# Kernel optimization log

Hardware: AMD Instinct MI355X
Metric: run time of the kernel (lower is better)

The kernel has to match this reference:

```python
import jax, jax.numpy as jnp
import numpy as np

B, S, E, H, D = 4, 2048, 1024, 16, 64


def setup_inputs() -> dict:
    key = jax.random.key(0)
    ks = jax.random.split(key, 6)
    scale_in = 1.0 / np.sqrt(E)
    return {
        "x": jax.random.normal(ks[0], (B, S, E), dtype=jnp.float32),
        "Wq": jax.random.normal(ks[1], (H, E, D), dtype=jnp.float32) * scale_in,
        "bq": jnp.zeros((H, D), dtype=jnp.float32),
        "Wk": jax.random.normal(ks[2], (H, E, D), dtype=jnp.float32) * scale_in,
        "bk": jnp.zeros((H, D), dtype=jnp.float32),
        "Wv": jax.random.normal(ks[3], (H, E, D), dtype=jnp.float32) * scale_in,
        "bv": jnp.zeros((H, D), dtype=jnp.float32),
        "Wo": jax.random.normal(ks[4], (H * D, E), dtype=jnp.float32) * (1.0 / np.sqrt(H * D)),
        "bo": jnp.zeros((E,), dtype=jnp.float32),
    }


def reference(x, Wq, bq, Wk, bk, Wv, bv, Wo, bo):
    # Per-head Q/K/V projections, batched over heads: [B,S,E] x [H,E,D] -> [B,H,S,D]
    q = jnp.einsum("bse,hed->bhsd", x, Wq) + bq[None, :, None, :]
    k = jnp.einsum("bse,hed->bhsd", x, Wk) + bk[None, :, None, :]
    v = jnp.einsum("bse,hed->bhsd", x, Wv) + bv[None, :, None, :]

    d = q.shape[-1]
    scores = jnp.einsum("bhqd,bhkd->bhqk", q, k) / jnp.sqrt(jnp.asarray(d, q.dtype))
    # Causal mask (registered tril buffer of size max_seq_len in HeadAttention)
    seq = scores.shape[-1]
    causal = jnp.tril(jnp.ones((seq, seq), dtype=bool))
    scores = jnp.where(causal[None, None, :, :], scores, jnp.asarray(-1e9, scores.dtype))
    attn = jax.nn.softmax(scores, axis=-1)
    out = jnp.einsum("bhqk,bhkd->bhqd", attn, v)  # [B,H,S,D]

    # Concat heads: [B,S,H*D], then output projection (dropout is identity in eval)
    out = out.transpose(0, 2, 1, 3).reshape(out.shape[0], out.shape[2], -1)
    return out @ Wo + bo
```

## Files before the change

kernel.cpp:

```cpp
#include <hip/hip_runtime.h>

typedef __bf16 bf16x8 __attribute__((ext_vector_type(8)));
typedef __bf16 bf16x4 __attribute__((ext_vector_type(4)));
typedef float  f32x4  __attribute__((ext_vector_type(4)));

#define B_    4
#define S_    2048
#define E_    1024
#define H_    16
#define D_    64
#define MROWS (B_*S_)

#define SCORE_SCALE 0.18033688011112043f

__device__ __forceinline__ void load_lds16(const void* g, void* l) {
  __builtin_amdgcn_global_load_lds((__attribute__((address_space(1))) void*)g,
                                   (__attribute__((address_space(3))) void*)l,
                                   16, 0, 0);
}

__device__ __forceinline__ f32x4 mfma16(bf16x8 a, bf16x8 b, f32x4 c) {
  return __builtin_amdgcn_mfma_f32_16x16x32_bf16(a, b, c, 0, 0, 0);
}

__device__ __forceinline__ int swz(int row, int dchunk) {
  return row * 64 + ((dchunk ^ (row & 7)) * 8);
}


__global__ void prep(const float4* __restrict__ x, const float* __restrict__ Wq,
                     const float* __restrict__ Wk, const float* __restrict__ Wv,
                     const float* __restrict__ bq, const float* __restrict__ bk,
                     const float* __restrict__ bv, const float* __restrict__ Wo,
                     __bf16* __restrict__ xb, __bf16* __restrict__ Wt,
                     float* __restrict__ bqkv, __bf16* __restrict__ Wot) {
  __shared__ float t[64][65];
  int bid = blockIdx.x;
  if (bid < 8192) {
    int id = bid * 256 + threadIdx.x;
    float4 v = x[id];
    bf16x4 o = { (__bf16)v.x, (__bf16)v.y, (__bf16)v.z, (__bf16)v.w };
    *(bf16x4*)(xb + 4 * (size_t)id) = o;
    return;
  }
  int tx = threadIdx.x & 63;
  int ty = threadIdx.x >> 6;
  if (bid < 8960) {
    int b2 = bid - 8192;
    int e0 = (b2 & 15) * 64;
    int h  = (b2 >> 4) & 15;
    int p  = b2 >> 8;
    const float* W    = (p == 0) ? Wq : (p == 1) ? Wk : Wv;
    const float* bsrc = (p == 0) ? bq : (p == 1) ? bk : bv;
#pragma unroll
    for (int r = 0; r < 16; ++r) {
      int eL = ty + r * 4;
      t[eL][tx] = W[((size_t)h * 1024 + (e0 + eL)) * 64 + tx];
    }
    __syncthreads();
#pragma unroll
    for (int r = 0; r < 16; ++r) {
      int d = ty + r * 4;
      Wt[((size_t)(p * 1024 + h * 64 + d)) * 1024 + e0 + tx] = (__bf16)t[tx][d];
    }
    if ((b2 & 15) == 0 && threadIdx.x < 64)
      bqkv[p * 1024 + h * 64 + threadIdx.x] = bsrc[h * 64 + threadIdx.x];
  } else {
    int b2 = bid - 8960;
    int hd0 = (b2 >> 4) * 64;
    int e0  = (b2 & 15) * 64;
#pragma unroll
    for (int r = 0; r < 16; ++r) {
      int hdL = ty + r * 4;
      t[hdL][tx] = Wo[(size_t)(hd0 + hdL) * 1024 + e0 + tx];
    }
    __syncthreads();
#pragma unroll
    for (int r = 0; r < 16; ++r) {
      int eL = ty + r * 4;
      Wot[(size_t)(e0 + eL) * 1024 + hd0 + tx] = (__bf16)t[tx][eL];
    }
  }
}


template <int MODE, int BN, int NDIM>
__global__ __launch_bounds__(512, 4) void gemm8h(const __bf16* __restrict__ A,
                                                 const __bf16* __restrict__ Bt,
                                                 const float* __restrict__ bias,
                                                 void* __restrict__ Cout,
                                                 __bf16* __restrict__ VT) {
  constexpr int K = 1024;
  constexpr int NB = BN / 64;
  constexpr int WC = BN / 4;
  __shared__ __attribute__((aligned(16))) __bf16 As[2 * 128 * 64];
  __shared__ __attribute__((aligned(16))) __bf16 Bs[2 * BN * 64];

  int tid = threadIdx.x, wave = tid >> 6, lane = tid & 63;
  int quad = lane >> 4, cc = lane & 15;
  constexpr int nb = NDIM / BN;
  int nwg = (int)gridDim.x;
  int bid = (int)blockIdx.x;
  bid = (bid & 7) * (nwg >> 3) + (bid >> 3);
  int bm = bid / nb, bn = bid % nb;
  const __bf16* Abase = A + (size_t)bm * 128 * K;
  const __bf16* Bbase = Bt + (size_t)bn * BN * K;
  int wrow = (wave >> 2) * 64;
  int wcol = (wave & 3) * WC;

  f32x4 acc[4][NB];
#pragma unroll
  for (int m = 0; m < 4; ++m)
#pragma unroll
    for (int n = 0; n < NB; ++n) acc[m][n] = (f32x4){0.f, 0.f, 0.f, 0.f};

  int srl = tid >> 3;
  int sch = tid & 7;
  int scol = (sch ^ (srl & 7)) * 8;

#define STAGE_A(t, sub, buf)                                                   \
  load_lds16(Abase + (size_t)((sub) * 64 + srl) * K + (t) * 64 + scol,         \
             &As[(buf) * 8192 + (sub) * 4096 + tid * 8])
#define STAGE_B(t, sub, buf)                                                   \
  load_lds16(Bbase + (size_t)((sub) * 64 + srl) * K + (t) * 64 + scol,         \
             &Bs[(buf) * (BN * 64) + (sub) * 4096 + tid * 8])

#pragma unroll
  for (int s = 0; s < 2; ++s) STAGE_A(0, s, 0);
#pragma unroll
  for (int s = 0; s < NB; ++s) STAGE_B(0, s, 0);
#pragma unroll
  for (int s = 0; s < 2; ++s) STAGE_A(1, s, 1);
  asm volatile("s_waitcnt vmcnt(2)" ::: "memory");
  __builtin_amdgcn_sched_barrier(0);
  asm volatile("s_barrier" ::: "memory");

  bf16x8 af[4][2], bfr[NB][2];

#define RD_B(buf)                                                              \
  _Pragma("unroll") for (int n = 0; n < NB; ++n)                               \
      _Pragma("unroll") for (int kk = 0; kk < 2; ++kk)                         \
          bfr[n][kk] = *(const bf16x8*)&Bs[(buf) * (BN * 64) +                 \
                                           swz(wcol + n * 16 + cc, kk * 4 + quad)]
#define RD_A2(buf, mlo)                                                        \
  _Pragma("unroll") for (int m = mlo; m < (mlo) + 2; ++m)                      \
      _Pragma("unroll") for (int kk = 0; kk < 2; ++kk)                         \
          af[m][kk] = *(const bf16x8*)&As[(buf) * 8192 +                       \
                                          swz(wrow + m * 16 + cc, kk * 4 + quad)]
#define MFMA_M(m)                                                              \
  do {                                                                         \
    __builtin_amdgcn_s_setprio(1);                                             \
    _Pragma("unroll") for (int n = 0; n < NB; ++n)                             \
        _Pragma("unroll") for (int kk = 0; kk < 2; ++kk)                       \
            acc[m][n] = mfma16(af[m][kk], bfr[n][kk], acc[m][n]);              \
    __builtin_amdgcn_s_setprio(0);                                             \
  } while (0)
#define LGKM0                                                                  \
  asm volatile("s_waitcnt lgkmcnt(0)" ::: "memory");                           \
  __builtin_amdgcn_sched_barrier(0)
#define VMC2                                                                   \
  asm volatile("s_waitcnt vmcnt(2)" ::: "memory");                             \
  __builtin_amdgcn_sched_barrier(0)
#define BAR asm volatile("s_barrier" ::: "memory")

#pragma unroll 1
  for (int it = 0; it < 8; ++it) {
    int b_t = 2 * it + 1;
    int c_t = (2 * it + 2) & 15;
    int d_t = (2 * it + 3) & 15;
    RD_B(0); RD_A2(0, 0);
    STAGE_B(b_t, 0, 1); STAGE_B(b_t, 1, 1);
    LGKM0; MFMA_M(0); BAR;
    RD_A2(0, 2);
    if (NB >= 3) STAGE_B(b_t, 2, 1);
    LGKM0; MFMA_M(1); BAR;
    STAGE_A(c_t, 0, 0); STAGE_A(c_t, 1, 0);
    MFMA_M(2); BAR;
    MFMA_M(3);
    VMC2; BAR;
    RD_B(1); RD_A2(1, 0);
    STAGE_B(c_t, 0, 0); STAGE_B(c_t, 1, 0);
    LGKM0; MFMA_M(0); BAR;
    RD_A2(1, 2);
    if (NB >= 3) STAGE_B(c_t, 2, 0);
    LGKM0; MFMA_M(1); BAR;
    STAGE_A(d_t, 0, 1); STAGE_A(d_t, 1, 1);
    MFMA_M(2); BAR;
    MFMA_M(3);
    VMC2; BAR;
  }
  asm volatile("s_waitcnt vmcnt(0)" ::: "memory");

#pragma unroll
  for (int n = 0; n < NB; ++n) {
    int gcol = bn * BN + wcol + n * 16 + cc;
    float bv = bias[gcol];
#pragma unroll
    for (int m = 0; m < 4; ++m) {
      int grow0 = bm * 128 + wrow + m * 16 + quad * 4;
      if (MODE == 0) {
#pragma unroll
        for (int r = 0; r < 4; ++r)
          ((float*)Cout)[(size_t)(grow0 + r) * NDIM + gcol] = acc[m][n][r] + bv;
      } else if (gcol < 2048) {
        float sc = (gcol < 1024) ? SCORE_SCALE : 1.0f;
#pragma unroll
        for (int r = 0; r < 4; ++r)
          ((__bf16*)Cout)[(size_t)(grow0 + r) * 2048 + gcol] =
              (__bf16)((acc[m][n][r] + bv) * sc);
      } else {
        int bh = (grow0 >> 11) * 16 + ((gcol >> 6) & 15);
        int d  = gcol & 63;
        bf16x4 pk;
#pragma unroll
        for (int r = 0; r < 4; ++r) pk[r] = (__bf16)(acc[m][n][r] + bv);
        *(bf16x4*)&VT[((size_t)(bh * 64 + d)) * 2048 + (grow0 & 2047)] = pk;
      }
    }
  }
#undef STAGE_A
#undef STAGE_B
#undef RD_B
#undef RD_A2
#undef MFMA_M
#undef LGKM0
#undef VMC2
#undef BAR
}


__global__ __launch_bounds__(256, 3) void attn(const __bf16* __restrict__ QKb,
                                               const __bf16* __restrict__ VT,
                                               __bf16* __restrict__ O) {
  int bx = blockIdx.x;
  int bh = bx & 63;
  int g  = bx >> 6;
  int qt = (g < 8) ? (15 - g) : (g - 8);
  int h  = bh & 15;
  int b  = bh >> 4;
  int q0 = qt * 128;
  int tid = threadIdx.x, wave = tid >> 6, lane = tid & 63;
  int quad = lane >> 4, c = lane & 15;

  __shared__ __attribute__((aligned(16))) __bf16 smem[24576];
  __bf16* Qs = smem;
  __bf16* Ks = smem + 8192;
  __bf16* Vs = smem + 16384;
  __bf16* Ps = smem + wave * 2048;

  const __bf16* Qbase = QKb + (size_t)(b * S_ + q0) * 2048 + h * 64;
  const __bf16* Vbase = VT + (size_t)bh * (64 * 2048);
#pragma unroll
  for (int p = 0; p < 4; ++p) {
    int gi = tid + p * 256;
    int row = gi >> 3, pch = gi & 7;
    load_lds16(Qbase + (size_t)row * 2048 + (pch ^ (row & 7)) * 8, &Qs[gi * 8]);
  }
  {
    const __bf16* Kb = QKb + (size_t)(b * S_) * 2048 + 1024 + h * 64;
#pragma unroll
    for (int p = 0; p < 2; ++p) {
      int gi = tid + p * 256;
      int row = gi >> 3, pch = gi & 7;
      load_lds16(Kb + (size_t)row * 2048 + (pch ^ (row & 7)) * 8, &Ks[gi * 8]);
      load_lds16(Vbase + (size_t)row * 2048 + (pch ^ (row & 7)) * 8, &Vs[gi * 8]);
    }
  }
  __syncthreads();

  bf16x8 qf[2][2];
#pragma unroll
  for (int i = 0; i < 2; ++i)
#pragma unroll
    for (int kk = 0; kk < 2; ++kk)
      qf[i][kk] = *(const bf16x8*)&Qs[swz(wave * 32 + i * 16 + c, kk * 4 + quad)];

  const __bf16 one_b = (__bf16)1.0f;
  bf16x8 ones = { one_b, one_b, one_b, one_b, one_b, one_b, one_b, one_b };

  f32x4 acc_o[2][4], acc_l[2];
#pragma unroll
  for (int i = 0; i < 2; ++i) {
    acc_l[i] = (f32x4){0.f, 0.f, 0.f, 0.f};
#pragma unroll
    for (int j = 0; j < 4; ++j) acc_o[i][j] = (f32x4){0.f, 0.f, 0.f, 0.f};
  }

  int qwave = q0 + wave * 32;
  int ntiles = qt * 2 + 2;
  for (int t = 0; t < ntiles; ++t) {
    int cur = t & 1;
    if (t + 1 < ntiles) {
      int kv1 = (t + 1) * 64;
      const __bf16* Kb = QKb + (size_t)(b * S_ + kv1) * 2048 + 1024 + h * 64;
      const __bf16* Vb = Vbase + kv1;
#pragma unroll
      for (int p = 0; p < 2; ++p) {
        int gi = tid + p * 256;
        int row = gi >> 3, pch = gi & 7;
        load_lds16(Kb + (size_t)row * 2048 + (pch ^ (row & 7)) * 8,
                   &Ks[(cur ^ 1) * 4096 + gi * 8]);
        load_lds16(Vb + (size_t)row * 2048 + (pch ^ (row & 7)) * 8,
                   &Vs[(cur ^ 1) * 4096 + gi * 8]);
      }
    }

    int kv0 = t * 64;
    if (kv0 <= qwave + 31) {
      const __bf16* Kc = Ks + cur * 4096;
      const __bf16* Vc = Vs + cur * 4096;

      f32x4 acc_t[2][4];
#pragma unroll
      for (int i = 0; i < 2; ++i)
#pragma unroll
        for (int j = 0; j < 4; ++j) acc_t[i][j] = (f32x4){0.f, 0.f, 0.f, 0.f};
      bf16x8 kf[4][2];
#pragma unroll
      for (int j = 0; j < 4; ++j)
#pragma unroll
        for (int kk = 0; kk < 2; ++kk)
          kf[j][kk] = *(const bf16x8*)&Kc[swz(j * 16 + c, kk * 4 + quad)];
      __builtin_amdgcn_s_setprio(1);
#pragma unroll
      for (int i = 0; i < 2; ++i)
#pragma unroll
        for (int j = 0; j < 4; ++j)
#pragma unroll
          for (int kk = 0; kk < 2; ++kk)
            acc_t[i][j] = mfma16(kf[j][kk], qf[i][kk], acc_t[i][j]);
      __builtin_amdgcn_s_setprio(0);

      bool domask = (kv0 + 63 > qwave);
#pragma unroll
      for (int i = 0; i < 2; ++i) {
        int q_l = i * 16 + c;
        int q_g = qwave + q_l;
#pragma unroll
        for (int j = 0; j < 4; ++j) {
          bf16x4 pk;
#pragma unroll
          for (int r = 0; r < 4; ++r) {
            float p = __builtin_amdgcn_exp2f(acc_t[i][j][r]);
            if (domask) {
              int kv = kv0 + j * 16 + quad * 4 + r;
              p = (kv > q_g) ? 0.f : p;
            }
            pk[r] = (__bf16)p;
          }
          int dch8 = j * 2 + (quad >> 1);
          int phys = q_l * 64 + ((dch8 ^ (q_l & 7)) * 8) + (quad & 1) * 4;
          *(bf16x4*)&Ps[phys] = pk;
        }
      }

      bf16x8 pf[2][2], vf[4][2];
#pragma unroll
      for (int i = 0; i < 2; ++i)
#pragma unroll
        for (int kk = 0; kk < 2; ++kk)
          pf[i][kk] = *(const bf16x8*)&Ps[swz(i * 16 + c, kk * 4 + quad)];
#pragma unroll
      for (int j = 0; j < 4; ++j)
#pragma unroll
        for (int kk = 0; kk < 2; ++kk)
          vf[j][kk] = *(const bf16x8*)&Vc[swz(j * 16 + c, kk * 4 + quad)];
      __builtin_amdgcn_s_setprio(1);
#pragma unroll
      for (int i = 0; i < 2; ++i) {
#pragma unroll
        for (int j = 0; j < 4; ++j)
#pragma unroll
          for (int kk = 0; kk < 2; ++kk)
            acc_o[i][j] = mfma16(pf[i][kk], vf[j][kk], acc_o[i][j]);
        acc_l[i] = mfma16(pf[i][0], ones, acc_l[i]);
        acc_l[i] = mfma16(pf[i][1], ones, acc_l[i]);
      }
      __builtin_amdgcn_s_setprio(0);
    }

    __syncthreads();
  }

  __bf16* Obase = O + (size_t)(b * S_ + q0) * 1024 + h * 64;
#pragma unroll
  for (int i = 0; i < 2; ++i)
#pragma unroll
    for (int r = 0; r < 4; ++r) {
      float rl = 1.0f / acc_l[i][r];
      int row = wave * 32 + i * 16 + quad * 4 + r;
#pragma unroll
      for (int j = 0; j < 4; ++j)
        Obase[(size_t)row * 1024 + j * 16 + c] = (__bf16)(acc_o[i][j][r] * rl);
    }
}


extern "C" void kernel_launch(void* const* d_in, const int* in_sizes, int n_in,
                              void* d_out, int out_size, void* d_ws, size_t ws_size,
                              hipStream_t stream) {
  (void)in_sizes; (void)n_in; (void)out_size; (void)ws_size;
  const float* x  = (const float*)d_in[0];
  const float* Wq = (const float*)d_in[1];
  const float* bq = (const float*)d_in[2];
  const float* Wk = (const float*)d_in[3];
  const float* bk = (const float*)d_in[4];
  const float* Wv = (const float*)d_in[5];
  const float* bv = (const float*)d_in[6];
  const float* Wo = (const float*)d_in[7];
  const float* bo = (const float*)d_in[8];

  char* w = (char*)d_ws;
  __bf16* xb   = (__bf16*)(w);
  __bf16* Wt   = (__bf16*)(w + (16ull << 20));
  __bf16* Wot  = (__bf16*)(w + (22ull << 20));
  float*  bqkv = (float*) (w + (24ull << 20));
  __bf16* QKb  = (__bf16*)(w + (25ull << 20));
  __bf16* Ob   = (__bf16*)(w + (57ull << 20));
  __bf16* VT   = (__bf16*)(w + (73ull << 20));

  prep<<<9216, 256, 0, stream>>>((const float4*)x, Wq, Wk, Wv, bq, bk, bv, Wo,
                                 xb, Wt, bqkv, Wot);
  gemm8h<1, 192, 3072><<<1024, 512, 0, stream>>>(xb, Wt, bqkv, (void*)QKb, VT);
  attn<<<1024, 256, 0, stream>>>(QKb, VT, Ob);
  gemm8h<0, 128, 1024><<<512, 512, 0, stream>>>(Ob, Wot, bo, d_out, nullptr);
}
```

Baseline: 242.5 us.

## Pair high and low causal query tiles in one 512-thread attention block

Each attention block now processes two 128-row query tiles, one near the end and its mirror near the start, with 8 waves sharing a single K/V stream through LDS. This halves the K/V global loads per query pair and balances causal work inside each block instead of across blocks. The trade-offs are more LDS per block, fewer blocks (512 instead of 1024), and waves on the low tile sitting idle for the later K/V tiles while still joining the barriers.

```diff
diff --git a/kernel.cpp b/kernel.cpp
--- a/kernel.cpp
+++ b/kernel.cpp
@@ -229,42 +229,42 @@
 }
 
 
-__global__ __launch_bounds__(256, 3) void attn(const __bf16* __restrict__ QKb,
+__global__ __launch_bounds__(512, 4) void attn(const __bf16* __restrict__ QKb,
                                                const __bf16* __restrict__ VT,
                                                __bf16* __restrict__ O) {
   int bx = blockIdx.x;
   int bh = bx & 63;
   int g  = bx >> 6;
-  int qt = (g < 8) ? (15 - g) : (g - 8);
+  int qth = 15 - g;
+  int qtl = g;
   int h  = bh & 15;
   int b  = bh >> 4;
-  int q0 = qt * 128;
+  int q0h = qth * 128, q0l = qtl * 128;
   int tid = threadIdx.x, wave = tid >> 6, lane = tid & 63;
   int quad = lane >> 4, c = lane & 15;
 
-  __shared__ __attribute__((aligned(16))) __bf16 smem[24576];
+  __shared__ __attribute__((aligned(16))) __bf16 smem[32768];
   __bf16* Qs = smem;
-  __bf16* Ks = smem + 8192;
-  __bf16* Vs = smem + 16384;
+  __bf16* Ks = smem + 16384;
+  __bf16* Vs = smem + 24576;
   __bf16* Ps = smem + wave * 2048;
 
-  const __bf16* Qbase = QKb + (size_t)(b * S_ + q0) * 2048 + h * 64;
+  const __bf16* Qbh = QKb + (size_t)(b * S_ + q0h) * 2048 + h * 64;
+  const __bf16* Qbl = QKb + (size_t)(b * S_ + q0l) * 2048 + h * 64;
   const __bf16* Vbase = VT + (size_t)bh * (64 * 2048);
 #pragma unroll
   for (int p = 0; p < 4; ++p) {
-    int gi = tid + p * 256;
+    int gi = tid + p * 512;
     int row = gi >> 3, pch = gi & 7;
-    load_lds16(Qbase + (size_t)row * 2048 + (pch ^ (row & 7)) * 8, &Qs[gi * 8]);
+    const __bf16* base = (p < 2) ? Qbh : Qbl;
+    load_lds16(base + (size_t)(row & 127) * 2048 + (pch ^ (row & 7)) * 8,
+               &Qs[gi * 8]);
   }
   {
     const __bf16* Kb = QKb + (size_t)(b * S_) * 2048 + 1024 + h * 64;
-#pragma unroll
-    for (int p = 0; p < 2; ++p) {
-      int gi = tid + p * 256;
-      int row = gi >> 3, pch = gi & 7;
-      load_lds16(Kb + (size_t)row * 2048 + (pch ^ (row & 7)) * 8, &Ks[gi * 8]);
-      load_lds16(Vbase + (size_t)row * 2048 + (pch ^ (row & 7)) * 8, &Vs[gi * 8]);
-    }
+    int row = tid >> 3, pch = tid & 7;
+    load_lds16(Kb + (size_t)row * 2048 + (pch ^ (row & 7)) * 8, &Ks[tid * 8]);
+    load_lds16(Vbase + (size_t)row * 2048 + (pch ^ (row & 7)) * 8, &Vs[tid * 8]);
   }
   __syncthreads();
 
@@ -286,23 +286,19 @@
     for (int j = 0; j < 4; ++j) acc_o[i][j] = (f32x4){0.f, 0.f, 0.f, 0.f};
   }
 
-  int qwave = q0 + wave * 32;
-  int ntiles = qt * 2 + 2;
+  int qwave = (wave < 4) ? (q0h + wave * 32) : (q0l + (wave - 4) * 32);
+  int ntiles = qth * 2 + 2;
   for (int t = 0; t < ntiles; ++t) {
     int cur = t & 1;
     if (t + 1 < ntiles) {
       int kv1 = (t + 1) * 64;
       const __bf16* Kb = QKb + (size_t)(b * S_ + kv1) * 2048 + 1024 + h * 64;
       const __bf16* Vb = Vbase + kv1;
-#pragma unroll
-      for (int p = 0; p < 2; ++p) {
-        int gi = tid + p * 256;
-        int row = gi >> 3, pch = gi & 7;
-        load_lds16(Kb + (size_t)row * 2048 + (pch ^ (row & 7)) * 8,
-                   &Ks[(cur ^ 1) * 4096 + gi * 8]);
-        load_lds16(Vb + (size_t)row * 2048 + (pch ^ (row & 7)) * 8,
-                   &Vs[(cur ^ 1) * 4096 + gi * 8]);
-      }
+      int row = tid >> 3, pch = tid & 7;
+      load_lds16(Kb + (size_t)row * 2048 + (pch ^ (row & 7)) * 8,
+                 &Ks[(cur ^ 1) * 4096 + tid * 8]);
+      load_lds16(Vb + (size_t)row * 2048 + (pch ^ (row & 7)) * 8,
+                 &Vs[(cur ^ 1) * 4096 + tid * 8]);
     }
 
     int kv0 = t * 64;
@@ -382,13 +378,13 @@
     __syncthreads();
   }
 
-  __bf16* Obase = O + (size_t)(b * S_ + q0) * 1024 + h * 64;
+  __bf16* Obase = O + (size_t)(b * S_ + qwave) * 1024 + h * 64;
 #pragma unroll
   for (int i = 0; i < 2; ++i)
 #pragma unroll
     for (int r = 0; r < 4; ++r) {
       float rl = 1.0f / acc_l[i][r];
-      int row = wave * 32 + i * 16 + quad * 4 + r;
+      int row = i * 16 + quad * 4 + r;
 #pragma unroll
       for (int j = 0; j < 4; ++j)
         Obase[(size_t)row * 1024 + j * 16 + c] = (__bf16)(acc_o[i][j][r] * rl);
@@ -422,6 +418,6 @@
   prep<<<9216, 256, 0, stream>>>((const float4*)x, Wq, Wk, Wv, bq, bk, bv, Wo,
                                  xb, Wt, bqkv, Wot);
   gemm8h<1, 192, 3072><<<1024, 512, 0, stream>>>(xb, Wt, bqkv, (void*)QKb, VT);
-  attn<<<1024, 256, 0, stream>>>(QKb, VT, Ob);
+  attn<<<512, 512, 0, stream>>>(QKb, VT, Ob);
   gemm8h<0, 128, 1024><<<512, 512, 0, stream>>>(Ob, Wot, bo, d_out, nullptr);
 }
```

After: 251.2 us. 1.04x slower.
